# Kernel tuning notes

Hardware: AMD Instinct MI355X
Metric: run time of the kernel (lower is better)

Reference implementation:

```python
import jax, jax.numpy as jnp
import numpy as np

N_NODES, N_FEAT, HIDDEN, N_EDGES, N_GRAPHS = 50000, 128, 64, 800000, 64
BN_EPS = 1e-5


def setup_inputs() -> dict:
    key = jax.random.key(0)
    ks = jax.random.split(key, 12)
    x = jax.random.normal(ks[0], (N_NODES, N_FEAT), jnp.float32)
    edge_index = jax.random.randint(ks[1], (2, N_EDGES), 0, N_NODES, jnp.int32)
    batch = jnp.sort(jax.random.randint(ks[2], (N_NODES,), 0, N_GRAPHS, jnp.int32))
    s_in = 1.0 / np.sqrt(N_FEAT)
    s_h = 1.0 / np.sqrt(HIDDEN)
    return {
        "x": x,
        "edge_index": edge_index,
        "batch": batch,
        "W_in": jax.random.normal(ks[3], (HIDDEN, N_FEAT), jnp.float32) * s_in,
        "W1": jax.random.normal(ks[4], (HIDDEN, N_FEAT), jnp.float32) * s_in,
        "b1": jnp.zeros((HIDDEN,), jnp.float32),
        "Ws": jax.random.normal(ks[5], (4, HIDDEN, HIDDEN), jnp.float32) * s_h,
        "bs": jnp.zeros((4, HIDDEN), jnp.float32),
        "bn_gamma": jnp.ones((5, HIDDEN), jnp.float32),
        "bn_beta": jnp.zeros((5, HIDDEN), jnp.float32),
        "bn_mean": jnp.zeros((5, HIDDEN), jnp.float32),
        "bn_var": jnp.ones((5, HIDDEN), jnp.float32),
        "lin_w": jax.random.normal(ks[6], (1, HIDDEN), jnp.float32) * s_h,
        "lin_b": jnp.zeros((1,), jnp.float32),
    }


def reference(x, edge_index, batch, W_in, W1, b1, Ws, bs, bn_gamma, bn_beta, bn_mean, bn_var, lin_w, lin_b):
    N = x.shape[0]
    # add self loops (GCNConv default), symmetric normalization D^-1/2 (A+I) D^-1/2
    loop = jnp.arange(N, dtype=edge_index.dtype)
    src = jnp.concatenate([edge_index[0], loop])  # [E+N]
    dst = jnp.concatenate([edge_index[1], loop])
    deg = jax.ops.segment_sum(jnp.ones_like(dst, jnp.float32), dst, num_segments=N)
    dinv = jax.lax.rsqrt(deg)  # deg >= 1 due to self-loops
    norm = dinv[src] * dinv[dst]  # [E+N]

    def gcn(h, W, b):
        h = h @ W.T                          # [N, H]
        msg = h[src] * norm[:, None]          # gather + edge scaling
        out = jax.ops.segment_sum(msg, dst, num_segments=N)  # scatter-add
        return out + b

    def bn(h, i):
        # eval-mode BatchNorm1d with running stats
        return (h - bn_mean[i]) * (bn_gamma[i] * jax.lax.rsqrt(bn_var[i] + BN_EPS)) + bn_beta[i]

    identity = x @ W_in.T  # input projection for residual
    # layer 1 (dropout = identity in eval)
    h = jax.nn.relu(bn(gcn(x, W1, b1), 0)) + identity
    # layers 2-4 with residual
    for i in range(3):
        h = jax.nn.relu(bn(gcn(h, Ws[i], bs[i]), i + 1)) + h
    # layer 5, no residual afterwards
    h = jax.nn.relu(bn(gcn(h, Ws[3], bs[3]), 4))

    # global mean pool over graphs
    sums = jax.ops.segment_sum(h, batch, num_segments=N_GRAPHS)
    cnts = jax.ops.segment_sum(jnp.ones((N,), jnp.float32), batch, num_segments=N_GRAPHS)
    pooled = sums / jnp.maximum(cnts, 1.0)[:, None]  # [G, H]
    return pooled @ lin_w.T + lin_b  # [G, 1]
```

## Files before the change

kernel.cpp:

```cpp
#include <hip/hip_runtime.h>
#include <hip/hip_fp16.h>

#define N_NODES 50000
#define N_FEAT  128
#define HID     64
#define N_EDGES 800000
#define N_GRAPHS 64
#define MAXDEG  64
#define BN_EPS  1e-5f
#define NB256(n) (((n) + 255) / 256)

__global__ __launch_bounds__(256) void k_zero(int* fill) {
    int i = blockIdx.x * 256 + threadIdx.x;
    if (i < N_NODES) fill[i] = 0;
}

#define GE_NB 2500
__global__ __launch_bounds__(256) void k_gemmedge(const int* __restrict__ ei,
                                                  int* fill, unsigned short* __restrict__ colp,
                                                  const float* __restrict__ x,
                                                  const float* __restrict__ W_in,
                                                  const float* __restrict__ W1,
                                                  float* __restrict__ h,
                                                  __half* __restrict__ g16) {
    __shared__ float4 Wt[2][8 * 65];
    __shared__ float4 xs[20 * 32];
    const int bid = blockIdx.x;
    const int t = threadIdx.x;

    const int ebase = bid * 320;
    int s1 = ei[ebase + t];
    int d1 = ei[N_EDGES + ebase + t];
    int k1 = atomicAdd(&fill[d1], 1);
    int s2 = 0, d2 = 0, k2 = MAXDEG;
    if (t < 64) {
        s2 = ei[ebase + 256 + t];
        d2 = ei[N_EDGES + ebase + 256 + t];
        k2 = atomicAdd(&fill[d2], 1);
    }

    const int base = bid * 20;
    const float4* xv = (const float4*)(x + (long long)base * N_FEAT);
    for (int i = t; i < 20 * 32; i += 256) xs[i] = xv[i];

    const float4* W0v = (const float4*)W_in;
    const float4* W1v = (const float4*)W1;
    const int hh = t & 63;
    const int ng = t >> 6;
    float4 a0[5], a1[5];
#pragma unroll
    for (int j = 0; j < 5; ++j) {
        a0[j] = make_float4(0.f, 0.f, 0.f, 0.f);
        a1[j] = make_float4(0.f, 0.f, 0.f, 0.f);
    }

    for (int c = 0; c < 32; c += 8) {
        __syncthreads();
        for (int i = t; i < 64 * 8; i += 256) {
            int h2 = i >> 3, k4 = i & 7;
            Wt[0][k4 * 65 + h2] = W0v[h2 * 32 + c + k4];
            Wt[1][k4 * 65 + h2] = W1v[h2 * 32 + c + k4];
        }
        __syncthreads();
#pragma unroll
        for (int k4 = 0; k4 < 8; ++k4) {
            float4 w0 = Wt[0][k4 * 65 + hh];
            float4 w1 = Wt[1][k4 * 65 + hh];
#pragma unroll
            for (int j = 0; j < 5; ++j) {
                float4 xx = xs[(ng + 4 * j) * 32 + c + k4];
                a0[j].x += w0.x * xx.x; a0[j].y += w0.y * xx.y;
                a0[j].z += w0.z * xx.z; a0[j].w += w0.w * xx.w;
                a1[j].x += w1.x * xx.x; a1[j].y += w1.y * xx.y;
                a1[j].z += w1.z * xx.z; a1[j].w += w1.w * xx.w;
            }
        }
    }
#pragma unroll
    for (int j = 0; j < 5; ++j) {
        int node = base + ng + 4 * j;
        h[node * HID + hh]   = a0[j].x + a0[j].y + a0[j].z + a0[j].w;
        g16[node * HID + hh] = __float2half(a1[j].x + a1[j].y + a1[j].z + a1[j].w);
    }

    if (k1 < MAXDEG) colp[d1 * MAXDEG + k1] = (unsigned short)s1;
    if (k2 < MAXDEG) colp[d2 * MAXDEG + k2] = (unsigned short)s2;
}

__device__ __forceinline__ void acc8s(const uint4 r, float* a, float s) {
    float2 f0 = __half22float2(*(const __half2*)&r.x);
    float2 f1 = __half22float2(*(const __half2*)&r.y);
    float2 f2 = __half22float2(*(const __half2*)&r.z);
    float2 f3 = __half22float2(*(const __half2*)&r.w);
    a[0] += s * f0.x; a[1] += s * f0.y; a[2] += s * f1.x; a[3] += s * f1.y;
    a[4] += s * f2.x; a[5] += s * f2.y; a[6] += s * f3.x; a[7] += s * f3.y;
}

template <bool NSCALE, bool DOGEMM>
__global__ __launch_bounds__(256) void k_gather_fused(const __half* __restrict__ gin,
                                                      const unsigned short* __restrict__ colp,
                                                      const int* __restrict__ fill,
                                                      const float* __restrict__ b,
                                                      const float* __restrict__ gamma,
                                                      const float* __restrict__ beta,
                                                      const float* __restrict__ mean,
                                                      const float* __restrict__ var,
                                                      const float4* __restrict__ res4,
                                                      float4* __restrict__ h4,
                                                      const float* __restrict__ W,
                                                      __half* __restrict__ gout) {
    __shared__ float4 Wt[DOGEMM ? 16 * 65 : 1];
    __shared__ float4 hrow[DOGEMM ? 8 * 16 : 1];

    const int t = threadIdx.x;
    const int wv = t >> 6;
    const int lane = t & 63;
    const int hh8 = lane & 7;
    const int sub = lane >> 3;
    const int nA = blockIdx.x * 8 + wv * 2;
    const int nB = nA + 1;

    if (DOGEMM) {
        const float4* Wv = (const float4*)W;
        for (int i = t; i < HID * 16; i += 256) {
            int h2 = i >> 4, k4 = i & 15;
            Wt[k4 * 65 + h2] = Wv[i];
        }
        __syncthreads();
    }

    const uint4* gv = (const uint4*)gin;
    int flA = fill[nA], flB = fill[nB];
    int degA = flA < MAXDEG ? flA : MAXDEG;
    int degB = flB < MAXDEG ? flB : MAXDEG;

    const int myn   = (lane < 32) ? nA : nB;
    const int myj   = lane & 31;
    const int mydeg = (lane < 32) ? degA : degB;
    const bool valid = (myj < mydeg);
    int call = valid ? (int)colp[myn * MAXDEG + myj] : myn;
    float sall;
    if (NSCALE) sall = valid ? rsqrtf((float)fill[call] + 1.0f) : 0.0f;
    else        sall = valid ? 1.0f : 0.0f;

    float aA[8], aB[8];
#pragma unroll
    for (int i = 0; i < 8; ++i) { aA[i] = 0.f; aB[i] = 0.f; }

    int dA32 = degA < 32 ? degA : 32;
    int dB32 = degB < 32 ? degB : 32;
    int nra = (dA32 + 7) >> 3;
    int nrb = (dB32 + 7) >> 3;
    int nr = nra > nrb ? nra : nrb;
#pragma unroll 4
    for (int r = 0; r < nr; ++r) {
        int j = r * 8 + sub;
        if (r < nra) {
            int c = __shfl(call, j);
            float s = __shfl(sall, j);
            acc8s(gv[c * 8 + hh8], aA, s);
        }
        if (r < nrb) {
            int c = __shfl(call, 32 + j);
            float s = __shfl(sall, 32 + j);
            acc8s(gv[c * 8 + hh8], aB, s);
        }
    }
    if (degA > 32) {
        for (int j = 32 + sub; j < degA; j += 8) {
            int c = (int)colp[nA * MAXDEG + j];
            float s = NSCALE ? rsqrtf((float)fill[c] + 1.0f) : 1.0f;
            acc8s(gv[c * 8 + hh8], aA, s);
        }
    }
    if (degB > 32) {
        for (int j = 32 + sub; j < degB; j += 8) {
            int c = (int)colp[nB * MAXDEG + j];
            float s = NSCALE ? rsqrtf((float)fill[c] + 1.0f) : 1.0f;
            acc8s(gv[c * 8 + hh8], aB, s);
        }
    }

#pragma unroll
    for (int m = 8; m <= 32; m <<= 1) {
#pragma unroll
        for (int i = 0; i < 8; ++i) { aA[i] += __shfl_xor(aA[i], m); aB[i] += __shfl_xor(aB[i], m); }
    }

    const float diA = rsqrtf((float)flA + 1.0f);
    const float diB = rsqrtf((float)flB + 1.0f);
    acc8s(gv[nA * 8 + hh8], aA, NSCALE ? diA : 1.0f);
    acc8s(gv[nB * 8 + hh8], aB, NSCALE ? diB : 1.0f);

    float4 b0 = ((const float4*)b)[hh8 * 2],     b1 = ((const float4*)b)[hh8 * 2 + 1];
    float4 g0 = ((const float4*)gamma)[hh8 * 2], g1 = ((const float4*)gamma)[hh8 * 2 + 1];
    float4 e0 = ((const float4*)beta)[hh8 * 2],  e1 = ((const float4*)beta)[hh8 * 2 + 1];
    float4 m0 = ((const float4*)mean)[hh8 * 2],  m1 = ((const float4*)mean)[hh8 * 2 + 1];
    float4 v0 = ((const float4*)var)[hh8 * 2],   v1 = ((const float4*)var)[hh8 * 2 + 1];

    float bb[8] = {b0.x, b0.y, b0.z, b0.w, b1.x, b1.y, b1.z, b1.w};
    float gg[8] = {g0.x, g0.y, g0.z, g0.w, g1.x, g1.y, g1.z, g1.w};
    float ee[8] = {e0.x, e0.y, e0.z, e0.w, e1.x, e1.y, e1.z, e1.w};
    float mm[8] = {m0.x, m0.y, m0.z, m0.w, m1.x, m1.y, m1.z, m1.w};
    float vv[8] = {v0.x, v0.y, v0.z, v0.w, v1.x, v1.y, v1.z, v1.w};

    float oA[8], oB[8];
#pragma unroll
    for (int i = 0; i < 8; ++i) {
        float sc = gg[i] * rsqrtf(vv[i] + BN_EPS);
        float vA = (aA[i] * diA + bb[i] - mm[i]) * sc + ee[i];
        float vB = (aB[i] * diB + bb[i] - mm[i]) * sc + ee[i];
        oA[i] = fmaxf(vA, 0.f);
        oB[i] = fmaxf(vB, 0.f);
    }
    if (res4) {
        float4 rA0 = res4[nA * 16 + hh8 * 2], rA1 = res4[nA * 16 + hh8 * 2 + 1];
        float4 rB0 = res4[nB * 16 + hh8 * 2], rB1 = res4[nB * 16 + hh8 * 2 + 1];
        oA[0] += rA0.x; oA[1] += rA0.y; oA[2] += rA0.z; oA[3] += rA0.w;
        oA[4] += rA1.x; oA[5] += rA1.y; oA[6] += rA1.z; oA[7] += rA1.w;
        oB[0] += rB0.x; oB[1] += rB0.y; oB[2] += rB0.z; oB[3] += rB0.w;
        oB[4] += rB1.x; oB[5] += rB1.y; oB[6] += rB1.z; oB[7] += rB1.w;
    }
    float4 loA = make_float4(oA[0], oA[1], oA[2], oA[3]);
    float4 hiA = make_float4(oA[4], oA[5], oA[6], oA[7]);
    float4 loB = make_float4(oB[0], oB[1], oB[2], oB[3]);
    float4 hiB = make_float4(oB[4], oB[5], oB[6], oB[7]);
    if (sub == 0) {
        h4[nA * 16 + hh8 * 2]     = loA;
        h4[nA * 16 + hh8 * 2 + 1] = hiA;
        h4[nB * 16 + hh8 * 2]     = loB;
        h4[nB * 16 + hh8 * 2 + 1] = hiB;
        if (DOGEMM) {
            hrow[(wv * 2) * 16 + hh8 * 2]         = loA;
            hrow[(wv * 2) * 16 + hh8 * 2 + 1]     = hiA;
            hrow[(wv * 2 + 1) * 16 + hh8 * 2]     = loB;
            hrow[(wv * 2 + 1) * 16 + hh8 * 2 + 1] = hiB;
        }
    }

    if (DOGEMM) {
        const int hh = lane;
        float4 accA = make_float4(0.f, 0.f, 0.f, 0.f);
        float4 accB = make_float4(0.f, 0.f, 0.f, 0.f);
#pragma unroll
        for (int k4 = 0; k4 < 16; ++k4) {
            float4 w = Wt[k4 * 65 + hh];
            float4 hA = hrow[(wv * 2) * 16 + k4];
            float4 hB = hrow[(wv * 2 + 1) * 16 + k4];
            accA.x += hA.x * w.x; accA.y += hA.y * w.y;
            accA.z += hA.z * w.z; accA.w += hA.w * w.w;
            accB.x += hB.x * w.x; accB.y += hB.y * w.y;
            accB.z += hB.z * w.z; accB.w += hB.w * w.w;
        }
        gout[nA * HID + hh] = __float2half((accA.x + accA.y + accA.z + accA.w) * diA);
        gout[nB * HID + hh] = __float2half((accB.x + accB.y + accB.z + accB.w) * diB);
    }
}

__device__ __forceinline__ int lowerb(const int* __restrict__ b, int val) {
    int lo = 0, hi = N_NODES;
    while (lo < hi) {
        int mid = (lo + hi) >> 1;
        if (b[mid] < val) lo = mid + 1; else hi = mid;
    }
    return lo;
}

__global__ __launch_bounds__(1024) void k_poolfinal(const float* __restrict__ h,
                                                    const int* __restrict__ batch,
                                                    const float* __restrict__ lin_w,
                                                    const float* __restrict__ lin_b,
                                                    float* __restrict__ out) {
    __shared__ float red[16][HID];
    int g = blockIdx.x;
    int w = threadIdx.x >> 6;
    int hh = threadIdx.x & 63;
    int start = lowerb(batch, g);
    int end = lowerb(batch, g + 1);
    int len = end - start;
    float acc = 0.f;
    for (int n = start + w; n < end; n += 16) acc += h[n * HID + hh];
    red[w][hh] = acc;
    __syncthreads();
    if (w == 0) {
        float s = 0.f;
#pragma unroll
        for (int i = 0; i < 16; ++i) s += red[i][hh];
        float c = fmaxf((float)len, 1.0f);
        float v = (s / c) * lin_w[hh];
#pragma unroll
        for (int off = 32; off > 0; off >>= 1) v += __shfl_down(v, off);
        if (hh == 0) out[g] = v + lin_b[0];
    }
}

extern "C" void kernel_launch(void* const* d_in, const int* in_sizes, int n_in,
                              void* d_out, int out_size, void* d_ws, size_t ws_size,
                              hipStream_t stream) {
    const float* x     = (const float*)d_in[0];
    const int*   ei    = (const int*)d_in[1];
    const int*   batch = (const int*)d_in[2];
    const float* W_in  = (const float*)d_in[3];
    const float* W1    = (const float*)d_in[4];
    const float* b1    = (const float*)d_in[5];
    const float* Ws    = (const float*)d_in[6];
    const float* bs_   = (const float*)d_in[7];
    const float* bn_g  = (const float*)d_in[8];
    const float* bn_b  = (const float*)d_in[9];
    const float* bn_m  = (const float*)d_in[10];
    const float* bn_v  = (const float*)d_in[11];
    const float* lin_w = (const float*)d_in[12];
    const float* lin_b = (const float*)d_in[13];
    float* out = (float*)d_out;

    char* q = (char*)d_ws;
    int*            fill = (int*)q;             q += (size_t)50048 * 4;
    unsigned short* colp = (unsigned short*)q;  q += (size_t)N_NODES * MAXDEG * 2;
    __half*         g16a = (__half*)q;          q += (size_t)N_NODES * HID * 2;
    __half*         g16b = (__half*)q;          q += (size_t)N_NODES * HID * 2;
    float*          h    = (float*)q;           q += (size_t)N_NODES * HID * 4;

    const int NB_N   = NB256(N_NODES);
    const int NB_GA2 = N_NODES / 8;
    float4* h4 = (float4*)h;

    k_zero<<<NB_N, 256, 0, stream>>>(fill);
    k_gemmedge<<<GE_NB, 256, 0, stream>>>(ei, fill, colp, x, W_in, W1, h, g16a);

    k_gather_fused<true, true><<<NB_GA2, 256, 0, stream>>>(
        g16a, colp, fill, b1, bn_g, bn_b, bn_m, bn_v,
        (const float4*)h, h4, Ws + 0 * HID * HID, g16b);

    k_gather_fused<false, true><<<NB_GA2, 256, 0, stream>>>(
        g16b, colp, fill, bs_ + 0 * HID,
        bn_g + 1 * HID, bn_b + 1 * HID, bn_m + 1 * HID, bn_v + 1 * HID,
        (const float4*)h, h4, Ws + 1 * HID * HID, g16a);

    k_gather_fused<false, true><<<NB_GA2, 256, 0, stream>>>(
        g16a, colp, fill, bs_ + 1 * HID,
        bn_g + 2 * HID, bn_b + 2 * HID, bn_m + 2 * HID, bn_v + 2 * HID,
        (const float4*)h, h4, Ws + 2 * HID * HID, g16b);

    k_gather_fused<false, true><<<NB_GA2, 256, 0, stream>>>(
        g16b, colp, fill, bs_ + 2 * HID,
        bn_g + 3 * HID, bn_b + 3 * HID, bn_m + 3 * HID, bn_v + 3 * HID,
        (const float4*)h, h4, Ws + 3 * HID * HID, g16a);

    k_gather_fused<false, false><<<NB_GA2, 256, 0, stream>>>(
        g16a, colp, fill, bs_ + 3 * HID,
        bn_g + 4 * HID, bn_b + 4 * HID, bn_m + 4 * HID, bn_v + 4 * HID,
        nullptr, h4, nullptr, nullptr);

    k_poolfinal<<<N_GRAPHS, 1024, 0, stream>>>(h, batch, lin_w, lin_b, out);
}
```

Baseline: 348.9 us.

## Remap gather to one 8-lane group per node and prefetch GEMM weights

The fused gather kernel now gives each node its own 8-lane group, so every block handles 32 nodes instead of 8. Each group walks its neighbour list four columns at a time with 64-bit index loads and four gathers in flight, which replaces the shuffle-based two-nodes-per-wave scheme and its cross-lane reduction. The per-block GEMM now reuses each weight read from shared memory across 8 nodes, and the first kernel prefetches weight tiles into registers ahead of each shared-memory stage. The cost is divergence when node degrees differ within a wave, more registers for the 8 accumulators, and loop exits that depend on the wave-wide maximum degree.

```diff
diff --git a/kernel.cpp b/kernel.cpp
--- a/kernel.cpp
+++ b/kernel.cpp
@@ -39,12 +39,19 @@
         k2 = atomicAdd(&fill[d2], 1);
     }
 
+    const float4* W0v = (const float4*)W_in;
+    const float4* W1v = (const float4*)W1;
+    const int h2a = t >> 3, k4a = t & 7;
+    const int h2b = h2a + 32;
+    float4 w0a = W0v[h2a * 32 + k4a];
+    float4 w1a = W1v[h2a * 32 + k4a];
+    float4 w0b = W0v[h2b * 32 + k4a];
+    float4 w1b = W1v[h2b * 32 + k4a];
+
     const int base = bid * 20;
     const float4* xv = (const float4*)(x + (long long)base * N_FEAT);
     for (int i = t; i < 20 * 32; i += 256) xs[i] = xv[i];
 
-    const float4* W0v = (const float4*)W_in;
-    const float4* W1v = (const float4*)W1;
     const int hh = t & 63;
     const int ng = t >> 6;
     float4 a0[5], a1[5];
@@ -56,10 +63,11 @@
 
     for (int c = 0; c < 32; c += 8) {
         __syncthreads();
-        for (int i = t; i < 64 * 8; i += 256) {
-            int h2 = i >> 3, k4 = i & 7;
-            Wt[0][k4 * 65 + h2] = W0v[h2 * 32 + c + k4];
-            Wt[1][k4 * 65 + h2] = W1v[h2 * 32 + c + k4];
+        Wt[0][k4a * 65 + h2a] = w0a;  Wt[1][k4a * 65 + h2a] = w1a;
+        Wt[0][k4a * 65 + h2b] = w0b;  Wt[1][k4a * 65 + h2b] = w1b;
+        if (c + 8 < 32) {
+            w0a = W0v[h2a * 32 + c + 8 + k4a]; w1a = W1v[h2a * 32 + c + 8 + k4a];
+            w0b = W0v[h2b * 32 + c + 8 + k4a]; w1b = W1v[h2b * 32 + c + 8 + k4a];
         }
         __syncthreads();
 #pragma unroll
@@ -110,15 +118,16 @@
                                                       const float* __restrict__ W,
                                                       __half* __restrict__ gout) {
     __shared__ float4 Wt[DOGEMM ? 16 * 65 : 1];
-    __shared__ float4 hrow[DOGEMM ? 8 * 16 : 1];
+    __shared__ float4 hrow[DOGEMM ? 32 * 17 : 1];
 
     const int t = threadIdx.x;
     const int wv = t >> 6;
     const int lane = t & 63;
     const int hh8 = lane & 7;
     const int sub = lane >> 3;
-    const int nA = blockIdx.x * 8 + wv * 2;
-    const int nB = nA + 1;
+    const int nl = wv * 8 + sub;
+    const int n = blockIdx.x * 32 + nl;
+    const bool nvalid = (n < N_NODES);
 
     if (DOGEMM) {
         const float4* Wv = (const float4*)W;
@@ -130,67 +139,37 @@
     }
 
     const uint4* gv = (const uint4*)gin;
-    int flA = fill[nA], flB = fill[nB];
-    int degA = flA < MAXDEG ? flA : MAXDEG;
-    int degB = flB < MAXDEG ? flB : MAXDEG;
-
-    const int myn   = (lane < 32) ? nA : nB;
-    const int myj   = lane & 31;
-    const int mydeg = (lane < 32) ? degA : degB;
-    const bool valid = (myj < mydeg);
-    int call = valid ? (int)colp[myn * MAXDEG + myj] : myn;
-    float sall;
-    if (NSCALE) sall = valid ? rsqrtf((float)fill[call] + 1.0f) : 0.0f;
-    else        sall = valid ? 1.0f : 0.0f;
-
-    float aA[8], aB[8];
-#pragma unroll
-    for (int i = 0; i < 8; ++i) { aA[i] = 0.f; aB[i] = 0.f; }
-
-    int dA32 = degA < 32 ? degA : 32;
-    int dB32 = degB < 32 ? degB : 32;
-    int nra = (dA32 + 7) >> 3;
-    int nrb = (dB32 + 7) >> 3;
-    int nr = nra > nrb ? nra : nrb;
-#pragma unroll 4
-    for (int r = 0; r < nr; ++r) {
-        int j = r * 8 + sub;
-        if (r < nra) {
-            int c = __shfl(call, j);
-            float s = __shfl(sall, j);
-            acc8s(gv[c * 8 + hh8], aA, s);
-        }
-        if (r < nrb) {
-            int c = __shfl(call, 32 + j);
-            float s = __shfl(sall, 32 + j);
-            acc8s(gv[c * 8 + hh8], aB, s);
-        }
-    }
-    if (degA > 32) {
-        for (int j = 32 + sub; j < degA; j += 8) {
-            int c = (int)colp[nA * MAXDEG + j];
-            float s = NSCALE ? rsqrtf((float)fill[c] + 1.0f) : 1.0f;
-            acc8s(gv[c * 8 + hh8], aA, s);
-        }
-    }
-    if (degB > 32) {
-        for (int j = 32 + sub; j < degB; j += 8) {
-            int c = (int)colp[nB * MAXDEG + j];
-            float s = NSCALE ? rsqrtf((float)fill[c] + 1.0f) : 1.0f;
-            acc8s(gv[c * 8 + hh8], aB, s);
-        }
-    }
-
-#pragma unroll
-    for (int m = 8; m <= 32; m <<= 1) {
-#pragma unroll
-        for (int i = 0; i < 8; ++i) { aA[i] += __shfl_xor(aA[i], m); aB[i] += __shfl_xor(aB[i], m); }
-    }
-
-    const float diA = rsqrtf((float)flA + 1.0f);
-    const float diB = rsqrtf((float)flB + 1.0f);
-    acc8s(gv[nA * 8 + hh8], aA, NSCALE ? diA : 1.0f);
-    acc8s(gv[nB * 8 + hh8], aB, NSCALE ? diB : 1.0f);
+    const int fl = nvalid ? fill[n] : 0;
+    const int deg = fl < MAXDEG ? fl : MAXDEG;
+
+    float a[8];
+#pragma unroll
+    for (int i = 0; i < 8; ++i) a[i] = 0.f;
+
+    const unsigned long long* cp4 =
+        (const unsigned long long*)(colp + (size_t)n * MAXDEG);
+
+    for (int rb = 0; rb < MAXDEG; rb += 4) {
+        if (!__any(rb < deg)) break;
+        if (rb < deg) {
+            unsigned long long cc = cp4[rb >> 2];
+            int c[4]; float s[4]; uint4 v[4];
+#pragma unroll
+            for (int k = 0; k < 4; ++k) {
+                bool pk = (rb + k) < deg;
+                c[k] = pk ? (int)((cc >> (16 * k)) & 0xFFFFull) : 0;
+                if (NSCALE) s[k] = pk ? rsqrtf((float)fill[c[k]] + 1.0f) : 0.0f;
+                else        s[k] = pk ? 1.0f : 0.0f;
+            }
+#pragma unroll
+            for (int k = 0; k < 4; ++k) v[k] = gv[(size_t)c[k] * 8 + hh8];
+#pragma unroll
+            for (int k = 0; k < 4; ++k) acc8s(v[k], a, s[k]);
+        }
+    }
+
+    const float di = rsqrtf((float)fl + 1.0f);
+    if (nvalid) acc8s(gv[(size_t)n * 8 + hh8], a, NSCALE ? di : 1.0f);
 
     float4 b0 = ((const float4*)b)[hh8 * 2],     b1 = ((const float4*)b)[hh8 * 2 + 1];
     float4 g0 = ((const float4*)gamma)[hh8 * 2], g1 = ((const float4*)gamma)[hh8 * 2 + 1];
@@ -204,56 +183,51 @@
     float mm[8] = {m0.x, m0.y, m0.z, m0.w, m1.x, m1.y, m1.z, m1.w};
     float vv[8] = {v0.x, v0.y, v0.z, v0.w, v1.x, v1.y, v1.z, v1.w};
 
-    float oA[8], oB[8];
+    float o[8];
 #pragma unroll
     for (int i = 0; i < 8; ++i) {
         float sc = gg[i] * rsqrtf(vv[i] + BN_EPS);
-        float vA = (aA[i] * diA + bb[i] - mm[i]) * sc + ee[i];
-        float vB = (aB[i] * diB + bb[i] - mm[i]) * sc + ee[i];
-        oA[i] = fmaxf(vA, 0.f);
-        oB[i] = fmaxf(vB, 0.f);
-    }
-    if (res4) {
-        float4 rA0 = res4[nA * 16 + hh8 * 2], rA1 = res4[nA * 16 + hh8 * 2 + 1];
-        float4 rB0 = res4[nB * 16 + hh8 * 2], rB1 = res4[nB * 16 + hh8 * 2 + 1];
-        oA[0] += rA0.x; oA[1] += rA0.y; oA[2] += rA0.z; oA[3] += rA0.w;
-        oA[4] += rA1.x; oA[5] += rA1.y; oA[6] += rA1.z; oA[7] += rA1.w;
-        oB[0] += rB0.x; oB[1] += rB0.y; oB[2] += rB0.z; oB[3] += rB0.w;
-        oB[4] += rB1.x; oB[5] += rB1.y; oB[6] += rB1.z; oB[7] += rB1.w;
-    }
-    float4 loA = make_float4(oA[0], oA[1], oA[2], oA[3]);
-    float4 hiA = make_float4(oA[4], oA[5], oA[6], oA[7]);
-    float4 loB = make_float4(oB[0], oB[1], oB[2], oB[3]);
-    float4 hiB = make_float4(oB[4], oB[5], oB[6], oB[7]);
-    if (sub == 0) {
-        h4[nA * 16 + hh8 * 2]     = loA;
-        h4[nA * 16 + hh8 * 2 + 1] = hiA;
-        h4[nB * 16 + hh8 * 2]     = loB;
-        h4[nB * 16 + hh8 * 2 + 1] = hiB;
-        if (DOGEMM) {
-            hrow[(wv * 2) * 16 + hh8 * 2]         = loA;
-            hrow[(wv * 2) * 16 + hh8 * 2 + 1]     = hiA;
-            hrow[(wv * 2 + 1) * 16 + hh8 * 2]     = loB;
-            hrow[(wv * 2 + 1) * 16 + hh8 * 2 + 1] = hiB;
-        }
+        o[i] = fmaxf((a[i] * di + bb[i] - mm[i]) * sc + ee[i], 0.f);
+    }
+    if (res4 != nullptr && nvalid) {
+        float4 r0 = res4[(size_t)n * 16 + hh8 * 2], r1 = res4[(size_t)n * 16 + hh8 * 2 + 1];
+        o[0] += r0.x; o[1] += r0.y; o[2] += r0.z; o[3] += r0.w;
+        o[4] += r1.x; o[5] += r1.y; o[6] += r1.z; o[7] += r1.w;
+    }
+    float4 lo = make_float4(o[0], o[1], o[2], o[3]);
+    float4 hi = make_float4(o[4], o[5], o[6], o[7]);
+    if (nvalid) {
+        h4[(size_t)n * 16 + hh8 * 2]     = lo;
+        h4[(size_t)n * 16 + hh8 * 2 + 1] = hi;
     }
 
     if (DOGEMM) {
+        hrow[nl * 17 + hh8 * 2]     = lo;
+        hrow[nl * 17 + hh8 * 2 + 1] = hi;
         const int hh = lane;
-        float4 accA = make_float4(0.f, 0.f, 0.f, 0.f);
-        float4 accB = make_float4(0.f, 0.f, 0.f, 0.f);
+        const int nb = blockIdx.x * 32 + wv * 8;
+        float4 acc[8];
+#pragma unroll
+        for (int s8 = 0; s8 < 8; ++s8) acc[s8] = make_float4(0.f, 0.f, 0.f, 0.f);
 #pragma unroll
         for (int k4 = 0; k4 < 16; ++k4) {
             float4 w = Wt[k4 * 65 + hh];
-            float4 hA = hrow[(wv * 2) * 16 + k4];
-            float4 hB = hrow[(wv * 2 + 1) * 16 + k4];
-            accA.x += hA.x * w.x; accA.y += hA.y * w.y;
-            accA.z += hA.z * w.z; accA.w += hA.w * w.w;
-            accB.x += hB.x * w.x; accB.y += hB.y * w.y;
-            accB.z += hB.z * w.z; accB.w += hB.w * w.w;
-        }
-        gout[nA * HID + hh] = __float2half((accA.x + accA.y + accA.z + accA.w) * diA);
-        gout[nB * HID + hh] = __float2half((accB.x + accB.y + accB.z + accB.w) * diB);
+#pragma unroll
+            for (int s8 = 0; s8 < 8; ++s8) {
+                float4 hv = hrow[(wv * 8 + s8) * 17 + k4];
+                acc[s8].x += hv.x * w.x; acc[s8].y += hv.y * w.y;
+                acc[s8].z += hv.z * w.z; acc[s8].w += hv.w * w.w;
+            }
+        }
+#pragma unroll
+        for (int s8 = 0; s8 < 8; ++s8) {
+            int ns = nb + s8;
+            if (ns < N_NODES) {
+                float dd = rsqrtf((float)fill[ns] + 1.0f);
+                gout[(size_t)ns * HID + hh] =
+                    __float2half((acc[s8].x + acc[s8].y + acc[s8].z + acc[s8].w) * dd);
+            }
+        }
     }
 }
 
@@ -320,33 +294,33 @@
     __half*         g16b = (__half*)q;          q += (size_t)N_NODES * HID * 2;
     float*          h    = (float*)q;           q += (size_t)N_NODES * HID * 4;
 
-    const int NB_N   = NB256(N_NODES);
-    const int NB_GA2 = N_NODES / 8;
+    const int NB_N  = NB256(N_NODES);
+    const int NB_GA = (N_NODES + 31) / 32;
     float4* h4 = (float4*)h;
 
     k_zero<<<NB_N, 256, 0, stream>>>(fill);
     k_gemmedge<<<GE_NB, 256, 0, stream>>>(ei, fill, colp, x, W_in, W1, h, g16a);
 
-    k_gather_fused<true, true><<<NB_GA2, 256, 0, stream>>>(
+    k_gather_fused<true, true><<<NB_GA, 256, 0, stream>>>(
         g16a, colp, fill, b1, bn_g, bn_b, bn_m, bn_v,
         (const float4*)h, h4, Ws + 0 * HID * HID, g16b);
 
-    k_gather_fused<false, true><<<NB_GA2, 256, 0, stream>>>(
+    k_gather_fused<false, true><<<NB_GA, 256, 0, stream>>>(
         g16b, colp, fill, bs_ + 0 * HID,
         bn_g + 1 * HID, bn_b + 1 * HID, bn_m + 1 * HID, bn_v + 1 * HID,
         (const float4*)h, h4, Ws + 1 * HID * HID, g16a);
 
-    k_gather_fused<false, true><<<NB_GA2, 256, 0, stream>>>(
+    k_gather_fused<false, true><<<NB_GA, 256, 0, stream>>>(
         g16a, colp, fill, bs_ + 1 * HID,
         bn_g + 2 * HID, bn_b + 2 * HID, bn_m + 2 * HID, bn_v + 2 * HID,
         (const float4*)h, h4, Ws + 2 * HID * HID, g16b);
 
-    k_gather_fused<false, true><<<NB_GA2, 256, 0, stream>>>(
+    k_gather_fused<false, true><<<NB_GA, 256, 0, stream>>>(
         g16b, colp, fill, bs_ + 2 * HID,
         bn_g + 3 * HID, bn_b + 3 * HID, bn_m + 3 * HID, bn_v + 3 * HID,
         (const float4*)h, h4, Ws + 3 * HID * HID, g16a);
 
-    k_gather_fused<false, false><<<NB_GA2, 256, 0, stream>>>(
+    k_gather_fused<false, false><<<NB_GA, 256, 0, stream>>>(
         g16a, colp, fill, bs_ + 3 * HID,
         bn_g + 4 * HID, bn_b + 4 * HID, bn_m + 4 * HID, bn_v + 4 * HID,
         nullptr, h4, nullptr, nullptr);
```

After: 643.2 us. 84.3% more time.
